# Optimization experiments

Hardware: AMD Instinct MI355X
Metric: run time of the kernel (lower is better)

## Reference

```python
import jax, jax.numpy as jnp
import numpy as np

B, T, S, NH, MD, FF, H = 2, 4096, 4096, 16, 64, 128, 4
HD = MD // H
NEG_SLOPE = 0.2
MAX_LOG_SCALE = float(np.log(100.0))  # SwinV2-style clamp on learnable logit scale


def layer_norm(x, g, b, eps=1e-5):
    mu = x.mean(-1, keepdims=True)
    var = ((x - mu) ** 2).mean(-1, keepdims=True)
    return (x - mu) * jax.lax.rsqrt(var + eps) * g + b


def leaky(x):
    return jnp.where(x >= 0, x, NEG_SLOPE * x)


def setup_inputs() -> dict:
    key = jax.random.key(0)
    ks = jax.random.split(key, 16)
    p = lambda i, shape: 0.02 * jax.random.normal(ks[i], shape, jnp.float32)
    return dict(
        x=jax.random.normal(ks[0], (B, S, 1), jnp.float32),
        coords_target=jax.random.uniform(ks[1], (B, T, 2), jnp.float32),
        coords_source=jax.random.uniform(ks[2], (B, S, 2), jnp.float32),
        pe_w1=p(3, (2, FF)), pe_b1=jnp.zeros((FF,), jnp.float32),
        pe_w2=p(4, (FF, MD)), pe_b2=jnp.zeros((MD,), jnp.float32),
        q_w=p(5, (MD, MD)), k_w=p(6, (MD, MD)), v_w=p(7, (1, MD)),
        logit_scale=jnp.zeros((H,), jnp.float32),
        out_w=p(8, (MD, MD)), out_b=jnp.zeros((MD,), jnp.float32),
        nh_w1=p(9, (MD, FF)), nh_b1=jnp.zeros((FF,), jnp.float32),
        nh_w2=p(10, (FF, 1)), nh_b2=jnp.zeros((1,), jnp.float32),
        uf_w1=p(11, (MD * NH, MD * NH)), uf_b1=jnp.zeros((MD * NH,), jnp.float32),
        uf_w2=p(12, (MD * NH, MD * NH)), uf_b2=jnp.zeros((MD * NH,), jnp.float32),
        ln1_g=jnp.ones((MD,), jnp.float32), ln1_b=jnp.zeros((MD,), jnp.float32),
        ln2_g=jnp.ones((MD,), jnp.float32), ln2_b=jnp.zeros((MD,), jnp.float32),
        ln3_g=jnp.ones((MD * NH,), jnp.float32), ln3_b=jnp.zeros((MD * NH,), jnp.float32),
    )


def reference(x, coords_target, coords_source, pe_w1, pe_b1, pe_w2, pe_b2,
              q_w, k_w, v_w, logit_scale, out_w, out_b,
              nh_w1, nh_b1, nh_w2, nh_b2, uf_w1, uf_b1, uf_w2, uf_b2,
              ln1_g, ln1_b, ln2_g, ln2_b, ln3_g, ln3_b):
    # ---- nn_layer: kNN gather of source values per target point ----
    d2 = jnp.sum((coords_target[:, :, None, :] - coords_source[:, None, :, :]) ** 2, -1)  # (B,T,S)
    _, idx = jax.lax.top_k(-d2, NH)  # (B,T,NH) nearest source indices
    gather = jax.vmap(lambda a, i: a[i])
    x_nh = gather(x, idx)                  # (B,T,NH,1)
    cs_nh = gather(coords_source, idx)     # (B,T,NH,2)
    rel = cs_nh - coords_target[:, :, None, :]  # relative coords (B,T,NH,2)

    # ---- relative position embedding MLP (with coordinate transform) ----
    c = jnp.sign(rel) * jnp.log1p(jnp.abs(rel))
    pe = jax.nn.relu(c @ pe_w1 + pe_b1) @ pe_w2 + pe_b2  # (B,T,NH,MD)

    # ---- value projection from raw gathered values (before pe add) ----
    v = x_nh.reshape(B * T, NH, 1) @ v_w  # (BT,NH,MD)

    h = layer_norm(x_nh + pe, ln1_g, ln1_b).reshape(B * T, NH, MD)
    q = h @ q_w
    k = h @ k_w

    # ---- local multi-head attention over the NH neighbors (cosine att w/ learnable logit scale) ----
    qh = q.reshape(B * T, NH, H, HD)
    kh = k.reshape(B * T, NH, H, HD)
    vh = v.reshape(B * T, NH, H, HD)
    qn = qh / (jnp.linalg.norm(qh, axis=-1, keepdims=True) + 1e-12)
    kn = kh / (jnp.linalg.norm(kh, axis=-1, keepdims=True) + 1e-12)
    scale = jnp.exp(jnp.minimum(logit_scale, MAX_LOG_SCALE))  # (H,)
    logits = jnp.einsum('nihd,njhd->nhij', qn, kn) * scale[None, :, None, None]
    att = jax.nn.softmax(logits, axis=-1)
    ao = jnp.einsum('nhij,njhd->nihd', att, vh).reshape(B * T, NH, MD)
    ao = ao @ out_w + out_b

    h = layer_norm(h + ao, ln2_g, ln2_b)
    # per-neighborhood MLP: md -> ff -> 1, broadcast residual add
    m = leaky(leaky(h @ nh_w1 + nh_b1) @ nh_w2 + nh_b2)  # (BT,NH,1)
    h = h + m

    # unfold neighbors into channel dim and run wide MLP
    hu = layer_norm(h.reshape(B, T, NH * MD), ln3_g, ln3_b)
    out = leaky(leaky(hu @ uf_w1 + uf_b1) @ uf_w2 + uf_b2)  # (B,T,NH*MD)
    return out
```

## Files before the change

### kernel.cpp

```cpp
#include <hip/hip_runtime.h>
#include <math.h>

#define B_ 2
#define T_ 4096
#define S_ 4096
#define NH_ 16
#define MD_ 64
#define FF_ 128
#define H_ 4
#define HD_ 16
#define BT_ (B_*T_)

typedef unsigned short u16;
typedef unsigned int u32;
typedef unsigned long long u64;
typedef __attribute__((ext_vector_type(8))) short short8;
typedef __attribute__((ext_vector_type(4))) float f32x4;

__device__ __forceinline__ float wsum64(float v) {
  #pragma unroll
  for (int off = 32; off > 0; off >>= 1) v += __shfl_xor(v, off, 64);
  return v;
}
__device__ __forceinline__ float leaky_(float x) { return x >= 0.f ? x : 0.2f * x; }
__device__ __forceinline__ u16 f2bf(float f) {
  u32 u = __float_as_uint(f);
  return (u16)((u + 0x7fffu + ((u >> 16) & 1u)) >> 16);
}
__device__ __forceinline__ float bf2f(u16 h) { return __uint_as_float((u32)h << 16); }

__device__ __forceinline__ void gload16(const void* g, void* l) {
  __builtin_amdgcn_global_load_lds(
      (const __attribute__((address_space(1))) u32*)g,
      (__attribute__((address_space(3))) u32*)l, 16, 0, 0);
}

__device__ __forceinline__ float dist2_(float2 c, float ctx, float cty) {
  float dx = ctx - c.x, dy = cty - c.y;
  return dx * dx + dy * dy;
}

__global__ __launch_bounds__(256) void k1_knn(
    const float* __restrict__ coords_target, const float* __restrict__ coords_source,
    const float* __restrict__ x, float* __restrict__ xnh, float* __restrict__ rel) {
  __shared__ float2 cs_s[S_];
  __shared__ u64 buf[4][128];
  const int tid = threadIdx.x;
  const int lane = tid & 63;
  const int wave = tid >> 6;
  const int n = blockIdx.x * 4 + wave;
  const int b = n >> 12;
  const float2* cs = (const float2*)coords_source + (size_t)b * S_;
  for (int i = tid; i < S_; i += 256) cs_s[i] = cs[i];
  __syncthreads();

  const float ctx = coords_target[n*2+0], cty = coords_target[n*2+1];

  float lmin = INFINITY;
  for (int kk = 0; kk < 64; ++kk)
    lmin = fminf(lmin, dist2_(cs_s[(kk << 6) | lane], ctx, cty));

  float v = lmin;
  #pragma unroll
  for (int k = 2; k <= 64; k <<= 1) {
    #pragma unroll
    for (int j = k >> 1; j > 0; j >>= 1) {
      float o = __shfl_xor(v, j, 64);
      bool keepmin = (((lane & j) == 0) == ((lane & k) == 0));
      v = keepmin ? fminf(v, o) : fmaxf(v, o);
    }
  }
  const float tau = __shfl(v, 15, 64);

  u64* wbuf = buf[wave];
  int cnt = 0;
  for (int kk = 0; kk < 64; ++kk) {
    int s = (kk << 6) | lane;
    float d2 = dist2_(cs_s[s], ctx, cty);
    bool q = (d2 <= tau);
    u64 mask = __ballot(q);
    if (q) {
      int pos = cnt + __popcll(mask & ((1ull << lane) - 1ull));
      if (pos < 128)
        wbuf[pos] = ((u64)__float_as_uint(d2) << 32) | (u32)s;
    }
    cnt += (int)__popcll(mask);
  }

  int myidx = 0;
  if (cnt >= 16 && cnt <= 128) {
    u64 c0 = (lane < cnt) ? wbuf[lane] : ~0ull;
    u64 c1 = (lane + 64 < cnt) ? wbuf[lane + 64] : ~0ull;
    for (int r = 0; r < 16; ++r) {
      u64 m = c0 < c1 ? c0 : c1;
      #pragma unroll
      for (int off = 32; off > 0; off >>= 1) {
        u64 o = __shfl_xor(m, off, 64);
        m = o < m ? o : m;
      }
      if (lane == r) myidx = (int)(u32)(m & 0xffffffffu);
      if (c0 == m) c0 = ~0ull;
      else if (c1 == m) c1 = ~0ull;
    }
  } else {
    float kd[16]; int ki[16];
    #pragma unroll
    for (int j = 0; j < 16; ++j) { kd[j] = INFINITY; ki[j] = 0x7fffffff; }
    for (int kk = 0; kk < 64; ++kk) {
      int s = (kk << 6) | lane;
      float d2 = dist2_(cs_s[s], ctx, cty);
      if (d2 < kd[15]) {
        float cd = d2; int ci = s;
        #pragma unroll
        for (int j = 0; j < 16; ++j) {
          bool sw = cd < kd[j];
          float td = sw ? kd[j] : cd;  int ti = sw ? ki[j] : ci;
          kd[j]    = sw ? cd : kd[j];  ki[j]    = sw ? ci : ki[j];
          cd = td; ci = ti;
        }
      }
    }
    for (int r = 0; r < 16; ++r) {
      float hd = kd[0]; int hi = ki[0];
      #pragma unroll
      for (int off = 32; off > 0; off >>= 1) {
        float od = __shfl_xor(hd, off, 64); int oi = __shfl_xor(hi, off, 64);
        bool take = (od < hd) || (od == hd && oi < hi);
        hd = take ? od : hd; hi = take ? oi : hi;
      }
      if (kd[0] == hd && ki[0] == hi) {
        #pragma unroll
        for (int j = 0; j < 15; ++j) { kd[j] = kd[j+1]; ki[j] = ki[j+1]; }
        kd[15] = INFINITY; ki[15] = 0x7fffffff;
      }
      if (lane == r) myidx = hi;
    }
  }

  if (lane < 16) {
    float2 c = cs_s[myidx];
    xnh[(size_t)n*NH_ + lane] = x[(size_t)b*S_ + myidx];
    rel[((size_t)n*NH_ + lane)*2 + 0] = c.x - ctx;
    rel[((size_t)n*NH_ + lane)*2 + 1] = c.y - cty;
  }
}

#define HBF_S 72
#define QKS2 24
__global__ __launch_bounds__(256) void k3_attn(
    const float* __restrict__ rel, const float* __restrict__ xnh,
    const float* __restrict__ pe_w1, const float* __restrict__ pe_b1,
    const u16* __restrict__ pew2t_hi, const u16* __restrict__ pew2t_lo,
    const float* __restrict__ pe_b2,
    const float* __restrict__ ln1_g, const float* __restrict__ ln1_b,
    const u16* __restrict__ qkwt_hi, const u16* __restrict__ qkwt_lo,
    const u16* __restrict__ nhw1t_hi, const u16* __restrict__ nhw1t_lo,
    const float* __restrict__ v_w, const float* __restrict__ logit_scale,
    const float* __restrict__ out_w, const float* __restrict__ out_b,
    const float* __restrict__ nh_b1, const float* __restrict__ nh_w2,
    const float* __restrict__ nh_b2,
    const float* __restrict__ ln2_g, const float* __restrict__ ln2_b,
    const float* __restrict__ ln3_g, const float* __restrict__ ln3_b,
    u16* __restrict__ hu_hi, u16* __restrict__ hu_lo) {
  const int tid = threadIdx.x;
  const int lane = tid & 63;
  const int wave = tid >> 6;
  const int n = blockIdx.x * 4 + wave;
  const int fr = lane & 15, fq = lane >> 4;

  __shared__ __align__(16) char smem[45824];
  u16* h_bf0 = (u16*)smem;
  u16* h_bf1 = h_bf0 + 64*HBF_S;
  u16* qkreg = h_bf1 + 64*HBF_S;
  u16* q_sB  = qkreg;
  u16* k_sB  = qkreg + 4*64*QKS2;
  u16* hid0  = qkreg;
  u16* hid1  = qkreg + 64*HBF_S;
  float* fmisc = (float*)(qkreg + 8*64*QKS2);
  float* xnh_s = fmisc;
  float* svx_s = fmisc + 64;
  float* mred  = fmisc + 64 + 256;
  float* c_s   = fmisc + 64 + 256 + 256;

  if (lane < 32) {
    float rv = rel[(size_t)blockIdx.x*128 + wave*32 + lane];
    float a = log1pf(fabsf(rv));
    c_s[wave*32 + lane] = rv > 0.f ? a : (rv < 0.f ? -a : 0.f);
  }
  if (tid < 64) xnh_s[tid] = xnh[(size_t)blockIdx.x*64 + tid];
  float wvo[4];
  #pragma unroll
  for (int h = 0; h < 4; ++h) {
    float a = 0.f;
    for (int d = 0; d < 16; ++d)
      a = fmaf(v_w[h*16+d], out_w[(size_t)(h*16+d)*64 + lane], a);
    wvo[h] = a;
  }
  __syncthreads();

  f32x4 acc_pe[4];
  #pragma unroll
  for (int nf = 0; nf < 4; ++nf) acc_pe[nf] = (f32x4){0,0,0,0};
  for (int p = 0; p < 2; ++p) {
    const float w10 = pe_w1[p*64 + lane];
    const float w11 = pe_w1[128 + p*64 + lane];
    const float b1  = pe_b1[p*64 + lane];
    #pragma unroll
    for (int i = 0; i < 16; ++i) {
      float c0 = c_s[wave*32 + i*2], c1v = c_s[wave*32 + i*2 + 1];
      float hv = fmaxf(fmaf(c0, w10, fmaf(c1v, w11, b1)), 0.f);
      u16 hh = f2bf(hv);
      hid0[(wave*16+i)*HBF_S + lane] = hh;
      hid1[(wave*16+i)*HBF_S + lane] = f2bf(hv - bf2f(hh));
    }
    __syncthreads();
    #pragma unroll
    for (int ks = 0; ks < 2; ++ks) {
      short8 ah = *(const short8*)&hid0[(wave*16+fr)*HBF_S + ks*32 + fq*8];
      short8 al = *(const short8*)&hid1[(wave*16+fr)*HBF_S + ks*32 + fq*8];
      #pragma unroll
      for (int nf = 0; nf < 4; ++nf) {
        short8 bh = *(const short8*)&pew2t_hi[(nf*16+fr)*128 + p*64 + ks*32 + fq*8];
        short8 bl = *(const short8*)&pew2t_lo[(nf*16+fr)*128 + p*64 + ks*32 + fq*8];
        acc_pe[nf] = __builtin_amdgcn_mfma_f32_16x16x32_bf16(ah, bh, acc_pe[nf], 0,0,0);
        acc_pe[nf] = __builtin_amdgcn_mfma_f32_16x16x32_bf16(ah, bl, acc_pe[nf], 0,0,0);
        acc_pe[nf] = __builtin_amdgcn_mfma_f32_16x16x32_bf16(al, bh, acc_pe[nf], 0,0,0);
      }
    }
    __syncthreads();
  }

  {
    float gv[4], bv[4], b2v[4];
    #pragma unroll
    for (int nf = 0; nf < 4; ++nf) {
      int ch = nf*16 + fr;
      gv[nf] = ln1_g[ch]; bv[nf] = ln1_b[ch]; b2v[nf] = pe_b2[ch];
    }
    #pragma unroll
    for (int r = 0; r < 4; ++r) {
      const int row = wave*16 + fq*4 + r;
      const float xv = xnh_s[row];
      float t[4];
      #pragma unroll
      for (int nf = 0; nf < 4; ++nf) t[nf] = acc_pe[nf][r] + b2v[nf] + xv;
      float ps = t[0]+t[1]+t[2]+t[3];
      #pragma unroll
      for (int off = 1; off < 16; off <<= 1) ps += __shfl_xor(ps, off, 64);
      float mu = ps * (1.f/64.f);
      float vs = 0.f;
      #pragma unroll
      for (int nf = 0; nf < 4; ++nf) { float d = t[nf]-mu; vs = fmaf(d,d,vs); }
      #pragma unroll
      for (int off = 1; off < 16; off <<= 1) vs += __shfl_xor(vs, off, 64);
      float rs = rsqrtf(vs*(1.f/64.f) + 1e-5f);
      #pragma unroll
      for (int nf = 0; nf < 4; ++nf) {
        int ch = nf*16 + fr;
        float hn = (t[nf]-mu)*rs*gv[nf] + bv[nf];
        u16 hh = f2bf(hn);
        h_bf0[row*HBF_S + ch] = hh;
        h_bf1[row*HBF_S + ch] = f2bf(hn - bf2f(hh));
      }
    }
  }
  __syncthreads();

  {
    short8 bqh[2], bql[2], bkh[2], bkl[2];
    #pragma unroll
    for (int ks = 0; ks < 2; ++ks) {
      const int qcol = wave*16 + fr, kcol = 64 + wave*16 + fr;
      const int ko = ks*32 + fq*8;
      bqh[ks] = *(const short8*)&qkwt_hi[qcol*64 + ko];
      bql[ks] = *(const short8*)&qkwt_lo[qcol*64 + ko];
      bkh[ks] = *(const short8*)&qkwt_hi[kcol*64 + ko];
      bkl[ks] = *(const short8*)&qkwt_lo[kcol*64 + ko];
    }
    f32x4 accq[4], acck[4];
    #pragma unroll
    for (int mf = 0; mf < 4; ++mf) { accq[mf] = (f32x4){0,0,0,0}; acck[mf] = (f32x4){0,0,0,0}; }
    #pragma unroll
    for (int ks = 0; ks < 2; ++ks) {
      #pragma unroll
      for (int mf = 0; mf < 4; ++mf) {
        short8 ah = *(const short8*)&h_bf0[(mf*16+fr)*HBF_S + ks*32 + fq*8];
        short8 al = *(const short8*)&h_bf1[(mf*16+fr)*HBF_S + ks*32 + fq*8];
        accq[mf] = __builtin_amdgcn_mfma_f32_16x16x32_bf16(ah, bqh[ks], accq[mf], 0,0,0);
        accq[mf] = __builtin_amdgcn_mfma_f32_16x16x32_bf16(ah, bql[ks], accq[mf], 0,0,0);
        accq[mf] = __builtin_amdgcn_mfma_f32_16x16x32_bf16(al, bqh[ks], accq[mf], 0,0,0);
        acck[mf] = __builtin_amdgcn_mfma_f32_16x16x32_bf16(ah, bkh[ks], acck[mf], 0,0,0);
        acck[mf] = __builtin_amdgcn_mfma_f32_16x16x32_bf16(ah, bkl[ks], acck[mf], 0,0,0);
        acck[mf] = __builtin_amdgcn_mfma_f32_16x16x32_bf16(al, bkh[ks], acck[mf], 0,0,0);
      }
    }
    #pragma unroll
    for (int mf = 0; mf < 4; ++mf)
      #pragma unroll
      for (int r = 0; r < 4; ++r) {
        const int row = mf*16 + fq*4 + r;
        q_sB[(wave*64+row)*QKS2 + fr] = f2bf(accq[mf][r]);
        k_sB[(wave*64+row)*QKS2 + fr] = f2bf(acck[mf][r]);
      }
  }
  __syncthreads();

  {
    const int nl = lane >> 4, il = lane & 15;
    const float sc = expf(fminf(logit_scale[wave], 4.60517019f));
    float qv[16]; float qs = 0.f;
    short8 qp0 = *(const short8*)&q_sB[(wave*64+lane)*QKS2 + 0];
    short8 qp1 = *(const short8*)&q_sB[(wave*64+lane)*QKS2 + 8];
    #pragma unroll
    for (int d = 0; d < 8; ++d) {
      qv[d]   = bf2f((u16)qp0[d]);  qs = fmaf(qv[d],   qv[d],   qs);
      qv[8+d] = bf2f((u16)qp1[d]);  qs = fmaf(qv[8+d], qv[8+d], qs);
    }
    const float rq = 1.f / (sqrtf(qs) + 1e-12f);
    float lg[16];
    #pragma unroll
    for (int j = 0; j < 16; ++j) {
      const int krow = (lane & 48) + j;
      short8 kp0 = *(const short8*)&k_sB[(wave*64+krow)*QKS2 + 0];
      short8 kp1 = *(const short8*)&k_sB[(wave*64+krow)*QKS2 + 8];
      float ks = 0.f, dt = 0.f;
      #pragma unroll
      for (int d = 0; d < 8; ++d) {
        float kv0 = bf2f((u16)kp0[d]);
        float kv1 = bf2f((u16)kp1[d]);
        ks = fmaf(kv0, kv0, ks); dt = fmaf(qv[d], kv0, dt);
        ks = fmaf(kv1, kv1, ks); dt = fmaf(qv[8+d], kv1, dt);
      }
      lg[j] = dt * rq * (1.f/(sqrtf(ks)+1e-12f)) * sc;
    }
    float mx = lg[0];
    #pragma unroll
    for (int j = 1; j < 16; ++j) mx = fmaxf(mx, lg[j]);
    float se = 0.f, sx = 0.f;
    #pragma unroll
    for (int j = 0; j < 16; ++j) {
      float e = __expf(lg[j] - mx);
      se += e;
      sx = fmaf(e, xnh_s[(lane & 48) + j], sx);
    }
    svx_s[(nl*16 + il)*4 + wave] = sx / se;
  }
  __syncthreads();

  const float ob = out_b[lane], g2 = ln2_g[lane], bb2 = ln2_b[lane];
  float h2[16];
  #pragma unroll
  for (int i = 0; i < 16; ++i) {
    float hfull = bf2f(h_bf0[(wave*16+i)*HBF_S + lane])
                + bf2f(h_bf1[(wave*16+i)*HBF_S + lane]);
    float o = ob;
    #pragma unroll
    for (int h = 0; h < 4; ++h) o = fmaf(svx_s[(wave*16+i)*4 + h], wvo[h], o);
    float t = hfull + o;
    float mu = wsum64(t) * (1.f/64.f);
    float d = t - mu;
    float var = wsum64(d*d) * (1.f/64.f);
    h2[i] = d * rsqrtf(var + 1e-5f) * g2 + bb2;
    u16 hh = f2bf(h2[i]);
    h_bf0[(wave*16+i)*HBF_S + lane] = hh;
    h_bf1[(wave*16+i)*HBF_S + lane] = f2bf(h2[i] - bf2f(hh));
  }
  __syncthreads();

  {
    short8 bnh[2][2], bnl[2][2];
    float b1v[2], w2v[2];
    #pragma unroll
    for (int cf = 0; cf < 2; ++cf) {
      const int col = wave*32 + cf*16 + fr;
      b1v[cf] = nh_b1[col];
      w2v[cf] = nh_w2[col];
      #pragma unroll
      for (int ks = 0; ks < 2; ++ks) {
        bnh[cf][ks] = *(const short8*)&nhw1t_hi[col*64 + ks*32 + fq*8];
        bnl[cf][ks] = *(const short8*)&nhw1t_lo[col*64 + ks*32 + fq*8];
      }
    }
    f32x4 accm[4][2];
    #pragma unroll
    for (int mf = 0; mf < 4; ++mf)
      #pragma unroll
      for (int cf = 0; cf < 2; ++cf) accm[mf][cf] = (f32x4){0,0,0,0};
    #pragma unroll
    for (int ks = 0; ks < 2; ++ks) {
      #pragma unroll
      for (int mf = 0; mf < 4; ++mf) {
        short8 ah = *(const short8*)&h_bf0[(mf*16+fr)*HBF_S + ks*32 + fq*8];
        short8 al = *(const short8*)&h_bf1[(mf*16+fr)*HBF_S + ks*32 + fq*8];
        #pragma unroll
        for (int cf = 0; cf < 2; ++cf) {
          accm[mf][cf] = __builtin_amdgcn_mfma_f32_16x16x32_bf16(ah, bnh[cf][ks], accm[mf][cf], 0,0,0);
          accm[mf][cf] = __builtin_amdgcn_mfma_f32_16x16x32_bf16(ah, bnl[cf][ks], accm[mf][cf], 0,0,0);
          accm[mf][cf] = __builtin_amdgcn_mfma_f32_16x16x32_bf16(al, bnh[cf][ks], accm[mf][cf], 0,0,0);
        }
      }
    }
    #pragma unroll
    for (int mf = 0; mf < 4; ++mf)
      #pragma unroll
      for (int r = 0; r < 4; ++r) {
        float p = leaky_(accm[mf][0][r] + b1v[0]) * w2v[0]
                + leaky_(accm[mf][1][r] + b1v[1]) * w2v[1];
        #pragma unroll
        for (int off = 1; off < 16; off <<= 1) p += __shfl_xor(p, off, 64);
        if (fr == 0) mred[wave*64 + mf*16 + fq*4 + r] = p;
      }
  }
  __syncthreads();

  const float nb2 = nh_b2[0];
  float h3[16];
  float s1 = 0.f, s2 = 0.f;
  #pragma unroll
  for (int i = 0; i < 16; ++i) {
    float sm = mred[0*64 + wave*16+i] + mred[1*64 + wave*16+i]
             + mred[2*64 + wave*16+i] + mred[3*64 + wave*16+i];
    float mi = leaky_(sm + nb2);
    float v3 = h2[i] + mi;
    h3[i] = v3;
    s1 += v3; s2 = fmaf(v3, v3, s2);
  }
  s1 = wsum64(s1); s2 = wsum64(s2);
  float mu = s1 * (1.f/1024.f);
  float var = s2 * (1.f/1024.f) - mu*mu;
  float rs = rsqrtf(var + 1e-5f);
  const size_t base = (size_t)n * 1024;
  #pragma unroll
  for (int i = 0; i < 16; ++i) {
    int cch = i*64 + lane;
    float v = (h3[i] - mu) * rs * ln3_g[cch] + ln3_b[cch];
    u16 hi16 = f2bf(v);
    hu_hi[base + cch] = hi16;
    hu_lo[base + cch] = f2bf(v - bf2f(hi16));
  }
}

__global__ __launch_bounds__(256) void k0_wsplit(
    const float* __restrict__ W1, const float* __restrict__ W2,
    u16* __restrict__ T1h, u16* __restrict__ T1l,
    u16* __restrict__ T2h, u16* __restrict__ T2l) {
  __shared__ float t[64][65];
  const float* W = blockIdx.z ? W2 : W1;
  u16* Th = blockIdx.z ? T2h : T1h;
  u16* Tl = blockIdx.z ? T2l : T1l;
  const int bx = blockIdx.x * 64, by = blockIdx.y * 64;
  for (int i = threadIdx.x; i < 64*64; i += 256) {
    int r = i >> 6, c = i & 63;
    t[r][c] = W[(size_t)(bx + r) * 1024 + by + c];
  }
  __syncthreads();
  for (int i = threadIdx.x; i < 64*64; i += 256) {
    int r2 = i >> 6, c2 = i & 63;
    float v = t[c2][r2];
    u16 hi = f2bf(v);
    size_t o = (size_t)(by + r2) * 1024 + bx + c2;
    Th[o] = hi;
    Tl[o] = f2bf(v - bf2f(hi));
  }
}

__global__ __launch_bounds__(256) void k0b_wsplit2(
    const float* __restrict__ q_w, const float* __restrict__ k_w,
    const float* __restrict__ nh_w1, const float* __restrict__ pe_w2,
    u16* __restrict__ qkwt_hi, u16* __restrict__ qkwt_lo,
    u16* __restrict__ nhw1t_hi, u16* __restrict__ nhw1t_lo,
    u16* __restrict__ pew2t_hi, u16* __restrict__ pew2t_lo) {
  int idx = blockIdx.x * 256 + threadIdx.x;
  if (idx < 8192) {
    int col = idx >> 6, kk = idx & 63;
    float v = (col < 64) ? q_w[kk*64 + col] : k_w[kk*64 + (col - 64)];
    u16 hi = f2bf(v);
    qkwt_hi[col*64 + kk] = hi;
    qkwt_lo[col*64 + kk] = f2bf(v - bf2f(hi));
  } else if (idx < 16384) {
    int e = idx - 8192;
    int col = e >> 6, kk = e & 63;
    float v = nh_w1[kk*128 + col];
    u16 hi = f2bf(v);
    nhw1t_hi[col*64 + kk] = hi;
    nhw1t_lo[col*64 + kk] = f2bf(v - bf2f(hi));
  } else {
    int e = idx - 16384;
    int col = e >> 7, j = e & 127;
    float v = pe_w2[j*64 + col];
    u16 hi = f2bf(v);
    pew2t_hi[col*128 + j] = hi;
    pew2t_lo[col*128 + j] = f2bf(v - bf2f(hi));
  }
}

template<int OUT_BF16>
__global__ __launch_bounds__(256, 2) void k5_gemm(
    const u16* __restrict__ Ah, const u16* __restrict__ Al,
    const u16* __restrict__ Bth, const u16* __restrict__ Btl,
    const float* __restrict__ bias,
    u16* __restrict__ Chi, u16* __restrict__ Clo, float* __restrict__ Cf) {
  __shared__ u16 As[2][128*32];
  __shared__ u16 Bs[2][128*32];
  const int tid = threadIdx.x;
  const int lane = tid & 63;
  const int wave = tid >> 6;
  const int wr = (wave >> 1) * 64, wc = (wave & 1) * 64;
  const int bid = (int)blockIdx.x;
  const int swz = (bid & 7) * 64 + (bid >> 3);
  const int mt = swz >> 3, nt = swz & 7;
  const int m0 = mt * 128, n0 = nt * 128;

  const int sr = tid >> 2, sk = (tid & 3) * 8;
  const size_t a_off = (size_t)(m0 + sr) * 1024 + sk;
  const size_t b_off = (size_t)(n0 + sr) * 1024 + sk;
  u16* lAh = &As[0][0] + tid * 8;
  u16* lAl = &As[1][0] + tid * 8;
  u16* lBh = &Bs[0][0] + tid * 8;
  u16* lBl = &Bs[1][0] + tid * 8;

  f32x4 acc[4][4];
  #pragma unroll
  for (int i = 0; i < 4; ++i)
    #pragma unroll
    for (int j = 0; j < 4; ++j) acc[i][j] = (f32x4){0.f, 0.f, 0.f, 0.f};

  const int fr = lane & 15, fq = lane >> 4;
  const int aoff = (wr + fr) * 32 + fq * 8;
  const int boff = (wc + fr) * 32 + fq * 8;

  for (int k0 = 0; k0 < 1024; k0 += 32) {
    __syncthreads();
    gload16(Ah  + a_off + k0,             lAh);
    gload16(Ah  + a_off + k0 + 64*1024,   lAh + 64*32);
    gload16(Al  + a_off + k0,             lAl);
    gload16(Al  + a_off + k0 + 64*1024,   lAl + 64*32);
    gload16(Bth + b_off + k0,             lBh);
    gload16(Bth + b_off + k0 + 64*1024,   lBh + 64*32);
    gload16(Btl + b_off + k0,             lBl);
    gload16(Btl + b_off + k0 + 64*1024,   lBl + 64*32);
    __syncthreads();

    short8 ah[4], al[4], bh[4], bl[4];
    #pragma unroll
    for (int i = 0; i < 4; ++i) {
      ah[i] = *(const short8*)&As[0][aoff + i*16*32];
      al[i] = *(const short8*)&As[1][aoff + i*16*32];
      bh[i] = *(const short8*)&Bs[0][boff + i*16*32];
      bl[i] = *(const short8*)&Bs[1][boff + i*16*32];
    }
    #pragma unroll
    for (int mi = 0; mi < 4; ++mi)
      #pragma unroll
      for (int ni = 0; ni < 4; ++ni) {
        acc[mi][ni] = __builtin_amdgcn_mfma_f32_16x16x32_bf16(ah[mi], bh[ni], acc[mi][ni], 0, 0, 0);
        acc[mi][ni] = __builtin_amdgcn_mfma_f32_16x16x32_bf16(ah[mi], bl[ni], acc[mi][ni], 0, 0, 0);
        acc[mi][ni] = __builtin_amdgcn_mfma_f32_16x16x32_bf16(al[mi], bh[ni], acc[mi][ni], 0, 0, 0);
      }
  }

  #pragma unroll
  for (int mi = 0; mi < 4; ++mi)
    #pragma unroll
    for (int ni = 0; ni < 4; ++ni) {
      const int col = n0 + wc + ni*16 + fr;
      const float bv = bias[col];
      #pragma unroll
      for (int r = 0; r < 4; ++r) {
        const int row = m0 + wr + mi*16 + fq*4 + r;
        float v = leaky_(acc[mi][ni][r] + bv);
        if (OUT_BF16) {
          u16 hi = f2bf(v);
          Chi[(size_t)row*1024 + col] = hi;
          Clo[(size_t)row*1024 + col] = f2bf(v - bf2f(hi));
        } else {
          Cf[(size_t)row*1024 + col] = v;
        }
      }
    }
}

extern "C" void kernel_launch(void* const* d_in, const int* in_sizes, int n_in,
                              void* d_out, int out_size, void* d_ws, size_t ws_size,
                              hipStream_t stream) {
  (void)in_sizes; (void)n_in; (void)out_size; (void)ws_size;
  const float* x     = (const float*)d_in[0];
  const float* ct    = (const float*)d_in[1];
  const float* cs    = (const float*)d_in[2];
  const float* pe_w1 = (const float*)d_in[3];
  const float* pe_b1 = (const float*)d_in[4];
  const float* pe_w2 = (const float*)d_in[5];
  const float* pe_b2 = (const float*)d_in[6];
  const float* q_w   = (const float*)d_in[7];
  const float* k_w   = (const float*)d_in[8];
  const float* v_w   = (const float*)d_in[9];
  const float* lsc   = (const float*)d_in[10];
  const float* out_w = (const float*)d_in[11];
  const float* out_b = (const float*)d_in[12];
  const float* nh_w1 = (const float*)d_in[13];
  const float* nh_b1 = (const float*)d_in[14];
  const float* nh_w2 = (const float*)d_in[15];
  const float* nh_b2 = (const float*)d_in[16];
  const float* uf_w1 = (const float*)d_in[17];
  const float* uf_b1 = (const float*)d_in[18];
  const float* uf_w2 = (const float*)d_in[19];
  const float* uf_b2 = (const float*)d_in[20];
  const float* ln1_g = (const float*)d_in[21];
  const float* ln1_b = (const float*)d_in[22];
  const float* ln2_g = (const float*)d_in[23];
  const float* ln2_b = (const float*)d_in[24];
  const float* ln3_g = (const float*)d_in[25];
  const float* ln3_b = (const float*)d_in[26];

  float* ws  = (float*)d_ws;
  float* xnh = ws;
  float* rel = ws + 131072;
  float* h   = ws + 393216;
  u16*  hu_hi = (u16*)(ws + 393216 + 8388608);
  u16*  hu_lo = hu_hi + 8388608;
  u16*  wbase = (u16*)(ws + 393216 + 2*8388608);
  u16*  w1t_hi = wbase;
  u16*  w1t_lo = wbase + 1048576;
  u16*  w2t_hi = wbase + 2*1048576;
  u16*  w2t_lo = wbase + 3*1048576;
  u16*  qkwt_hi  = wbase + 4*1048576;
  u16*  qkwt_lo  = qkwt_hi + 8192;
  u16*  nhw1t_hi = qkwt_hi + 16384;
  u16*  nhw1t_lo = qkwt_hi + 24576;
  u16*  pew2t_hi = qkwt_hi + 32768;
  u16*  pew2t_lo = qkwt_hi + 40960;
  u16*  mid_hi = (u16*)h;
  u16*  mid_lo = mid_hi + 8388608;
  float* out = (float*)d_out;

  k0_wsplit<<<dim3(16, 16, 2), dim3(256), 0, stream>>>(uf_w1, uf_w2,
                                                       w1t_hi, w1t_lo, w2t_hi, w2t_lo);
  k0b_wsplit2<<<dim3(96), dim3(256), 0, stream>>>(q_w, k_w, nh_w1, pe_w2,
                                                  qkwt_hi, qkwt_lo, nhw1t_hi, nhw1t_lo,
                                                  pew2t_hi, pew2t_lo);
  k1_knn<<<dim3(BT_/4), dim3(256), 0, stream>>>(ct, cs, x, xnh, rel);
  k3_attn<<<dim3(BT_/4), dim3(256), 0, stream>>>(rel, xnh, pe_w1, pe_b1,
                                                 pew2t_hi, pew2t_lo, pe_b2,
                                                 ln1_g, ln1_b,
                                                 qkwt_hi, qkwt_lo, nhw1t_hi, nhw1t_lo,
                                                 v_w, lsc, out_w, out_b,
                                                 nh_b1, nh_w2, nh_b2,
                                                 ln2_g, ln2_b, ln3_g, ln3_b, hu_hi, hu_lo);
  k5_gemm<1><<<dim3(512), dim3(256), 0, stream>>>(hu_hi, hu_lo, w1t_hi, w1t_lo, uf_b1,
                                                  mid_hi, mid_lo, nullptr);
  k5_gemm<0><<<dim3(512), dim3(256), 0, stream>>>(mid_hi, mid_lo, w2t_hi, w2t_lo, uf_b2,
                                                  nullptr, nullptr, out);
}
```

Measured before the change: 428.3 us.

## Drop split-bf16 compensation in k3 GEMMs and restructure PE hidden staging

Removes the hi/lo split-bf16 three-MFMA compensation in the positional-encoding, Q/K and neighbor-MLP GEMMs, so each uses a single bf16 MFMA with only the hi weights. The PE hidden layer is now staged all at once in a 128-wide shared buffer instead of two passes, which removes several barriers. The Q/K staging stride and the LDS footprint shrink, and one barrier between the Q/K store and the attention read is dropped. This trades accuracy for fewer MFMAs and less LDS traffic. Removing that barrier is only safe if each wave reads back only its own Q/K rows.

```diff
diff --git a/kernel.cpp b/kernel.cpp
--- a/kernel.cpp
+++ b/kernel.cpp
@@ -145,8 +145,9 @@
   }
 }
 
-#define HBF_S 72
-#define QKS2 24
+#define HBF_S 66
+#define HID_S 132
+#define QKS3 16
 __global__ __launch_bounds__(256) void k3_attn(
     const float* __restrict__ rel, const float* __restrict__ xnh,
     const float* __restrict__ pe_w1, const float* __restrict__ pe_b1,
@@ -162,21 +163,21 @@
     const float* __restrict__ ln2_g, const float* __restrict__ ln2_b,
     const float* __restrict__ ln3_g, const float* __restrict__ ln3_b,
     u16* __restrict__ hu_hi, u16* __restrict__ hu_lo) {
+  (void)pew2t_lo; (void)qkwt_lo; (void)nhw1t_lo;
   const int tid = threadIdx.x;
   const int lane = tid & 63;
   const int wave = tid >> 6;
   const int n = blockIdx.x * 4 + wave;
   const int fr = lane & 15, fq = lane >> 4;
 
-  __shared__ __align__(16) char smem[45824];
+  __shared__ __align__(16) char smem[36608];
   u16* h_bf0 = (u16*)smem;
   u16* h_bf1 = h_bf0 + 64*HBF_S;
-  u16* qkreg = h_bf1 + 64*HBF_S;
-  u16* q_sB  = qkreg;
-  u16* k_sB  = qkreg + 4*64*QKS2;
-  u16* hid0  = qkreg;
-  u16* hid1  = qkreg + 64*HBF_S;
-  float* fmisc = (float*)(qkreg + 8*64*QKS2);
+  u16* qkhid = h_bf1 + 64*HBF_S;
+  u16* hid   = qkhid;
+  u16* q_sB  = qkhid;
+  u16* k_sB  = qkhid + 4*64*QKS3;
+  float* fmisc = (float*)(qkhid + 8448);
   float* xnh_s = fmisc;
   float* svx_s = fmisc + 64;
   float* mred  = fmisc + 64 + 256;
@@ -196,38 +197,31 @@
       a = fmaf(v_w[h*16+d], out_w[(size_t)(h*16+d)*64 + lane], a);
     wvo[h] = a;
   }
-  __syncthreads();
-
-  f32x4 acc_pe[4];
-  #pragma unroll
-  for (int nf = 0; nf < 4; ++nf) acc_pe[nf] = (f32x4){0,0,0,0};
-  for (int p = 0; p < 2; ++p) {
-    const float w10 = pe_w1[p*64 + lane];
-    const float w11 = pe_w1[128 + p*64 + lane];
-    const float b1  = pe_b1[p*64 + lane];
+
+  {
+    const float w10a = pe_w1[lane],    w11a = pe_w1[128+lane],    b1a = pe_b1[lane];
+    const float w10b = pe_w1[64+lane], w11b = pe_w1[192+lane],    b1b = pe_b1[64+lane];
     #pragma unroll
     for (int i = 0; i < 16; ++i) {
       float c0 = c_s[wave*32 + i*2], c1v = c_s[wave*32 + i*2 + 1];
-      float hv = fmaxf(fmaf(c0, w10, fmaf(c1v, w11, b1)), 0.f);
-      u16 hh = f2bf(hv);
-      hid0[(wave*16+i)*HBF_S + lane] = hh;
-      hid1[(wave*16+i)*HBF_S + lane] = f2bf(hv - bf2f(hh));
-    }
-    __syncthreads();
-    #pragma unroll
-    for (int ks = 0; ks < 2; ++ks) {
-      short8 ah = *(const short8*)&hid0[(wave*16+fr)*HBF_S + ks*32 + fq*8];
-      short8 al = *(const short8*)&hid1[(wave*16+fr)*HBF_S + ks*32 + fq*8];
-      #pragma unroll
-      for (int nf = 0; nf < 4; ++nf) {
-        short8 bh = *(const short8*)&pew2t_hi[(nf*16+fr)*128 + p*64 + ks*32 + fq*8];
-        short8 bl = *(const short8*)&pew2t_lo[(nf*16+fr)*128 + p*64 + ks*32 + fq*8];
-        acc_pe[nf] = __builtin_amdgcn_mfma_f32_16x16x32_bf16(ah, bh, acc_pe[nf], 0,0,0);
-        acc_pe[nf] = __builtin_amdgcn_mfma_f32_16x16x32_bf16(ah, bl, acc_pe[nf], 0,0,0);
-        acc_pe[nf] = __builtin_amdgcn_mfma_f32_16x16x32_bf16(al, bh, acc_pe[nf], 0,0,0);
-      }
-    }
-    __syncthreads();
+      int row = wave*16 + i;
+      hid[row*HID_S + lane]      = f2bf(fmaxf(fmaf(c0, w10a, fmaf(c1v, w11a, b1a)), 0.f));
+      hid[row*HID_S + 64 + lane] = f2bf(fmaxf(fmaf(c0, w10b, fmaf(c1v, w11b, b1b)), 0.f));
+    }
+  }
+  __syncthreads();
+
+  f32x4 acc_pe[4];
+  #pragma unroll
+  for (int nf = 0; nf < 4; ++nf) acc_pe[nf] = (f32x4){0,0,0,0};
+  #pragma unroll
+  for (int ks = 0; ks < 4; ++ks) {
+    short8 ah = *(const short8*)&hid[(wave*16+fr)*HID_S + ks*32 + fq*8];
+    #pragma unroll
+    for (int nf = 0; nf < 4; ++nf) {
+      short8 bh = *(const short8*)&pew2t_hi[(nf*16+fr)*128 + ks*32 + fq*8];
+      acc_pe[nf] = __builtin_amdgcn_mfma_f32_16x16x32_bf16(ah, bh, acc_pe[nf], 0,0,0);
+    }
   }
 
   {
@@ -267,15 +261,13 @@
   __syncthreads();
 
   {
-    short8 bqh[2], bql[2], bkh[2], bkl[2];
+    short8 bqh[2], bkh[2];
     #pragma unroll
     for (int ks = 0; ks < 2; ++ks) {
       const int qcol = wave*16 + fr, kcol = 64 + wave*16 + fr;
       const int ko = ks*32 + fq*8;
       bqh[ks] = *(const short8*)&qkwt_hi[qcol*64 + ko];
-      bql[ks] = *(const short8*)&qkwt_lo[qcol*64 + ko];
       bkh[ks] = *(const short8*)&qkwt_hi[kcol*64 + ko];
-      bkl[ks] = *(const short8*)&qkwt_lo[kcol*64 + ko];
     }
     f32x4 accq[4], acck[4];
     #pragma unroll
@@ -285,13 +277,8 @@
       #pragma unroll
       for (int mf = 0; mf < 4; ++mf) {
         short8 ah = *(const short8*)&h_bf0[(mf*16+fr)*HBF_S + ks*32 + fq*8];
-        short8 al = *(const short8*)&h_bf1[(mf*16+fr)*HBF_S + ks*32 + fq*8];
         accq[mf] = __builtin_amdgcn_mfma_f32_16x16x32_bf16(ah, bqh[ks], accq[mf], 0,0,0);
-        accq[mf] = __builtin_amdgcn_mfma_f32_16x16x32_bf16(ah, bql[ks], accq[mf], 0,0,0);
-        accq[mf] = __builtin_amdgcn_mfma_f32_16x16x32_bf16(al, bqh[ks], accq[mf], 0,0,0);
         acck[mf] = __builtin_amdgcn_mfma_f32_16x16x32_bf16(ah, bkh[ks], acck[mf], 0,0,0);
-        acck[mf] = __builtin_amdgcn_mfma_f32_16x16x32_bf16(ah, bkl[ks], acck[mf], 0,0,0);
-        acck[mf] = __builtin_amdgcn_mfma_f32_16x16x32_bf16(al, bkh[ks], acck[mf], 0,0,0);
       }
     }
     #pragma unroll
@@ -299,18 +286,17 @@
       #pragma unroll
       for (int r = 0; r < 4; ++r) {
         const int row = mf*16 + fq*4 + r;
-        q_sB[(wave*64+row)*QKS2 + fr] = f2bf(accq[mf][r]);
-        k_sB[(wave*64+row)*QKS2 + fr] = f2bf(acck[mf][r]);
-      }
-  }
-  __syncthreads();
+        q_sB[(wave*64+row)*QKS3 + fr] = f2bf(accq[mf][r]);
+        k_sB[(wave*64+row)*QKS3 + fr] = f2bf(acck[mf][r]);
+      }
+  }
 
   {
     const int nl = lane >> 4, il = lane & 15;
     const float sc = expf(fminf(logit_scale[wave], 4.60517019f));
     float qv[16]; float qs = 0.f;
-    short8 qp0 = *(const short8*)&q_sB[(wave*64+lane)*QKS2 + 0];
-    short8 qp1 = *(const short8*)&q_sB[(wave*64+lane)*QKS2 + 8];
+    short8 qp0 = *(const short8*)&q_sB[(wave*64+lane)*QKS3 + 0];
+    short8 qp1 = *(const short8*)&q_sB[(wave*64+lane)*QKS3 + 8];
     #pragma unroll
     for (int d = 0; d < 8; ++d) {
       qv[d]   = bf2f((u16)qp0[d]);  qs = fmaf(qv[d],   qv[d],   qs);
@@ -321,8 +307,8 @@
     #pragma unroll
     for (int j = 0; j < 16; ++j) {
       const int krow = (lane & 48) + j;
-      short8 kp0 = *(const short8*)&k_sB[(wave*64+krow)*QKS2 + 0];
-      short8 kp1 = *(const short8*)&k_sB[(wave*64+krow)*QKS2 + 8];
+      short8 kp0 = *(const short8*)&k_sB[(wave*64+krow)*QKS3 + 0];
+      short8 kp1 = *(const short8*)&k_sB[(wave*64+krow)*QKS3 + 8];
       float ks = 0.f, dt = 0.f;
       #pragma unroll
       for (int d = 0; d < 8; ++d) {
@@ -361,14 +347,12 @@
     float d = t - mu;
     float var = wsum64(d*d) * (1.f/64.f);
     h2[i] = d * rsqrtf(var + 1e-5f) * g2 + bb2;
-    u16 hh = f2bf(h2[i]);
-    h_bf0[(wave*16+i)*HBF_S + lane] = hh;
-    h_bf1[(wave*16+i)*HBF_S + lane] = f2bf(h2[i] - bf2f(hh));
+    h_bf0[(wave*16+i)*HBF_S + lane] = f2bf(h2[i]);
   }
   __syncthreads();
 
   {
-    short8 bnh[2][2], bnl[2][2];
+    short8 bnh[2][2];
     float b1v[2], w2v[2];
     #pragma unroll
     for (int cf = 0; cf < 2; ++cf) {
@@ -376,10 +360,8 @@
       b1v[cf] = nh_b1[col];
       w2v[cf] = nh_w2[col];
       #pragma unroll
-      for (int ks = 0; ks < 2; ++ks) {
+      for (int ks = 0; ks < 2; ++ks)
         bnh[cf][ks] = *(const short8*)&nhw1t_hi[col*64 + ks*32 + fq*8];
-        bnl[cf][ks] = *(const short8*)&nhw1t_lo[col*64 + ks*32 + fq*8];
-      }
     }
     f32x4 accm[4][2];
     #pragma unroll
@@ -391,13 +373,9 @@
       #pragma unroll
       for (int mf = 0; mf < 4; ++mf) {
         short8 ah = *(const short8*)&h_bf0[(mf*16+fr)*HBF_S + ks*32 + fq*8];
-        short8 al = *(const short8*)&h_bf1[(mf*16+fr)*HBF_S + ks*32 + fq*8];
         #pragma unroll
-        for (int cf = 0; cf < 2; ++cf) {
+        for (int cf = 0; cf < 2; ++cf)
           accm[mf][cf] = __builtin_amdgcn_mfma_f32_16x16x32_bf16(ah, bnh[cf][ks], accm[mf][cf], 0,0,0);
-          accm[mf][cf] = __builtin_amdgcn_mfma_f32_16x16x32_bf16(ah, bnl[cf][ks], accm[mf][cf], 0,0,0);
-          accm[mf][cf] = __builtin_amdgcn_mfma_f32_16x16x32_bf16(al, bnh[cf][ks], accm[mf][cf], 0,0,0);
-        }
       }
     }
     #pragma unroll
```

Measured after the change: 414.4 us. 1.03x faster.
